# Optimization experiments

Hardware: AMD Instinct MI355X
Metric: run time of the kernel (lower is better)

The kernel has to match this reference:

```python
import jax, jax.numpy as jnp
import numpy as np

EMBED_DIM = 256
N_LEVELS = 4
N_HEADS = 8
N_POINTS = 4
HEAD_DIM = EMBED_DIM // N_HEADS
N_QUERIES = 8192
BATCH = 2
LEVEL_SHAPES = np.array([[128, 128], [64, 64], [32, 32], [16, 16]], dtype=np.int32)
HMAX, WMAX = 128, 128
EPS = 1e-5


def setup_inputs() -> dict:
    key = jax.random.key(0)
    ks = jax.random.split(key, 10)
    scale = 1.0 / np.sqrt(EMBED_DIM)
    query = jax.random.normal(ks[0], (N_QUERIES, EMBED_DIM), jnp.float32)
    xy_reference_points = jax.random.uniform(ks[1], (N_QUERIES, 2), jnp.float32, 0.05, 0.95)
    val = jax.random.normal(ks[2], (BATCH, HMAX, WMAX, N_LEVELS, EMBED_DIM), jnp.float32)
    # zero outside each level's valid support (mimics sparse COO: absent entries read as 0)
    hh = jnp.arange(HMAX)[:, None, None]
    ww = jnp.arange(WMAX)[None, :, None]
    lh = jnp.asarray(LEVEL_SHAPES[:, 0])[None, None, :]
    lw = jnp.asarray(LEVEL_SHAPES[:, 1])[None, None, :]
    mask = ((hh < lh) & (ww < lw)).astype(jnp.float32)
    stacked_value_tensors = val * mask[None, :, :, :, None]
    return {
        "query": query,
        "xy_reference_points": xy_reference_points,
        "stacked_value_tensors": stacked_value_tensors,
        "W_off": (jax.random.normal(ks[3], (EMBED_DIM, N_LEVELS * N_POINTS * N_HEADS * 2)) * scale * 0.1).astype(jnp.float32),
        "b_off": (jax.random.normal(ks[4], (N_LEVELS * N_POINTS * N_HEADS * 2,)) * 0.5).astype(jnp.float32),
        "W_attn": (jax.random.normal(ks[5], (EMBED_DIM, N_LEVELS * N_POINTS * N_HEADS)) * scale).astype(jnp.float32),
        "b_attn": jnp.zeros((N_LEVELS * N_POINTS * N_HEADS,), jnp.float32),
        "W_out": (jax.random.normal(ks[6], (EMBED_DIM, EMBED_DIM)) * scale).astype(jnp.float32),
        "b_out": jnp.zeros((EMBED_DIM,), jnp.float32),
        "batch_offsets": jnp.array([0, N_QUERIES // 2], jnp.int32),
        "spatial_shapes": jnp.asarray(LEVEL_SHAPES, jnp.int32),
    }


def reference(query, xy_reference_points, stacked_value_tensors, W_off, b_off,
              W_attn, b_attn, W_out, b_out, batch_offsets, spatial_shapes):
    Q = query.shape[0]
    # sampling offsets & attention weights (torch Linear with W stored [in,out])
    off = (query @ W_off + b_off).reshape(Q, N_LEVELS, N_POINTS, N_HEADS, 2)
    aw = (query @ W_attn + b_attn).reshape(Q, N_LEVELS * N_POINTS, N_HEADS)
    aw = jax.nn.softmax(aw, axis=1).reshape(Q, N_LEVELS, N_POINTS, N_HEADS)
    # sampling locations: sigmoid(inverse_sigmoid(ref) + offsets), then map (0,1)->(-1,1)
    r = jnp.clip(xy_reference_points, 0.0, 1.0)
    inv = jnp.log(jnp.clip(r, EPS, 1.0) / jnp.clip(1.0 - r, EPS, 1.0))
    loc = jax.nn.sigmoid(inv[:, None, None, None, :] + off) * 2.0 - 1.0  # (Q,L,P,H,2)
    # per-query batch index from batch_offsets (start index per batch element)
    bidx = jnp.searchsorted(batch_offsets, jnp.arange(Q), side="right") - 1  # (Q,)
    b = bidx[:, None, None, None]
    h_sz = spatial_shapes[:, 0].astype(loc.dtype)[None, :, None, None]
    w_sz = spatial_shapes[:, 1].astype(loc.dtype)[None, :, None, None]
    x = ((loc[..., 0] + 1.0) * w_sz - 1.0) / 2.0  # (Q,L,P,H)
    y = ((loc[..., 1] + 1.0) * h_sz - 1.0) / 2.0
    x0 = jnp.floor(x).astype(jnp.int32); x1 = x0 + 1
    y0 = jnp.floor(y).astype(jnp.int32); y1 = y0 + 1
    wcap = (spatial_shapes[:, 1] - 1).astype(jnp.int32)[None, :, None, None]
    hcap = (spatial_shapes[:, 0] - 1).astype(jnp.int32)[None, :, None, None]
    x0 = jnp.clip(x0, 0, wcap); x1 = jnp.clip(x1, 0, wcap)
    y0 = jnp.clip(y0, 0, hcap); y1 = jnp.clip(y1, 0, hcap)
    x0f = x0.astype(x.dtype); x1f = x1.astype(x.dtype)
    y0f = y0.astype(y.dtype); y1f = y1.astype(y.dtype)
    wa = (x1f - x) * (y1f - y)  # pairs with (x0,y0), as in source
    wb = (x1f - x) * (y - y0f)  # (x0,y1)
    wc = (x - x0f) * (y1f - y)  # (x1,y0)
    wd = (x - x0f) * (y - y0f)  # (x1,y1)
    V = stacked_value_tensors.reshape(BATCH, HMAX, WMAX, N_LEVELS, N_HEADS, HEAD_DIM)
    l = jnp.arange(N_LEVELS)[None, :, None, None]
    h = jnp.arange(N_HEADS)[None, None, None, :]
    # NOTE: source indexes (batch, x, y, level, head) -> x indexes the height dim; levels are square
    def g(xi, yi):
        return V[b, xi, yi, l, h]  # (Q,L,P,H,HEAD_DIM)
    sampled = (wa[..., None] * g(x0, y0) + wb[..., None] * g(x0, y1)
               + wc[..., None] * g(x1, y0) + wd[..., None] * g(x1, y1))
    out = jnp.einsum("qlphd,qlph->qhd", sampled, aw).reshape(Q, EMBED_DIM)
    return out @ W_out + b_out
```

## Files before the change

kernel.cpp:

```cpp
#include <hip/hip_runtime.h>
#include <math.h>

#define ED      256
#define NL      4
#define NH      8
#define NP      4
#define HD      32
#define HMAX    128
#define WMAX    128
#define NLP     16
#define NC      128
#define NOFF_AW 384
#define QPB     4
#define NBK     1024
#define BSTRIDE (HMAX*WMAX*NL*ED)
#define XSTRIDE (WMAX*NL*ED)
#define YSTRIDE (NL*ED)

typedef __attribute__((ext_vector_type(8))) __fp16   f16x8;
typedef __attribute__((ext_vector_type(4))) __fp16   f16x4;
typedef __attribute__((ext_vector_type(4))) float    f32x4;

__global__ __launch_bounds__(1024) void msda_sort_kernel(
    const float* __restrict__ refp,
    const int*   __restrict__ batch_off,
    int n_batch,
    int* __restrict__ bucket_of,
    int* __restrict__ perm,
    int nq)
{
    __shared__ int cnt[NBK];
    __shared__ int scan[NBK];
    const int t = threadIdx.x;
    cnt[t] = 0;
    __syncthreads();

    const int iters = (nq + 1023) >> 10;
    for (int i = 0; i < iters; ++i) {
        int q = i * 1024 + t;
        if (q < nq) {
            int b = 0;
            for (int j = 1; j < n_batch; ++j)
                if (batch_off[j] <= q) b = j;
            b = min(b, 3);
            float rx = refp[q * 2 + 0], ry = refp[q * 2 + 1];
            int bx = min(15, max(0, (int)(rx * 16.f)));
            int by = min(15, max(0, (int)(ry * 16.f)));
            int bk = (b << 8) | (by << 4) | bx;
            bucket_of[q] = bk;
            atomicAdd(&cnt[bk], 1);
        }
    }
    __syncthreads();

    scan[t] = cnt[t];
    __syncthreads();
    for (int d = 1; d < NBK; d <<= 1) {
        int v = scan[t];
        int u = (t >= d) ? scan[t - d] : 0;
        __syncthreads();
        scan[t] = v + u;
        __syncthreads();
    }
    cnt[t] = scan[t] - cnt[t];
    __syncthreads();

    for (int i = 0; i < iters; ++i) {
        int q = i * 1024 + t;
        if (q < nq) {
            int bk = bucket_of[q];
            int pos = atomicAdd(&cnt[bk], 1);
            perm[pos] = q;
        }
    }
}

__global__ __launch_bounds__(256) void msda_wconv_kernel(
    const float* __restrict__ W_off,
    const float* __restrict__ W_attn,
    const float* __restrict__ W_out,
    __fp16* __restrict__ WcatT,
    __fp16* __restrict__ WoutT)
{
    const int idx = blockIdx.x * 256 + threadIdx.x;
    const int t2 = NOFF_AW * ED;
    const int t3 = ED * ED;
    if (idx < t2) {
        int c = idx >> 8, e = idx & 255;
        float v = (c < ED) ? W_off[e * ED + c] : W_attn[e * NC + (c - ED)];
        WcatT[idx] = (__fp16)v;
    } else if (idx < t2 + t3) {
        int i = idx - t2;
        int c = i >> 8, e = i & 255;
        WoutT[i] = (__fp16)W_out[e * ED + c];
    }
}

__global__ __launch_bounds__(256) void gemm_f16_kernel(
    const float*  __restrict__ A,
    const __fp16* __restrict__ BT,
    const float* __restrict__ bias0,
    const float* __restrict__ bias1,
    float* __restrict__ C,
    int M, int NTOT, int bias_split)
{
    const int wave = threadIdx.x >> 6;
    const int lane = threadIdx.x & 63;
    const int gw   = blockIdx.x * 4 + wave;
    const int ngroups = NTOT >> 6;
    const int mg = gw / ngroups, ng = gw % ngroups;
    const int m16 = mg * 16, n64 = ng * 64;
    if (m16 >= M) return;

    const int mrow = lane & 15;
    const int quad = lane >> 4;

    const float4* Arow = (const float4*)(A + (size_t)(m16 + mrow) * 256 + quad * 8);
    const f16x8* B0 = (const f16x8*)(BT + (size_t)(n64 +  0 + mrow) * 256 + quad * 8);
    const f16x8* B1 = (const f16x8*)(BT + (size_t)(n64 + 16 + mrow) * 256 + quad * 8);
    const f16x8* B2 = (const f16x8*)(BT + (size_t)(n64 + 32 + mrow) * 256 + quad * 8);
    const f16x8* B3 = (const f16x8*)(BT + (size_t)(n64 + 48 + mrow) * 256 + quad * 8);

    f32x4 acc0 = {0.f,0.f,0.f,0.f}, acc1 = acc0, acc2 = acc0, acc3 = acc0;
    #pragma unroll
    for (int kb = 0; kb < 8; ++kb) {
        float4 a0 = Arow[kb * 8 + 0];
        float4 a1 = Arow[kb * 8 + 1];
        float av[8] = {a0.x, a0.y, a0.z, a0.w, a1.x, a1.y, a1.z, a1.w};
        f16x8 ah, al;
        #pragma unroll
        for (int j = 0; j < 8; ++j) {
            __fp16 h = (__fp16)av[j];
            ah[j] = h;
            al[j] = (__fp16)(av[j] - (float)h);
        }
        f16x8 b0 = B0[kb * 4], b1 = B1[kb * 4], b2 = B2[kb * 4], b3 = B3[kb * 4];
        acc0 = __builtin_amdgcn_mfma_f32_16x16x32_f16(ah, b0, acc0, 0, 0, 0);
        acc1 = __builtin_amdgcn_mfma_f32_16x16x32_f16(ah, b1, acc1, 0, 0, 0);
        acc2 = __builtin_amdgcn_mfma_f32_16x16x32_f16(ah, b2, acc2, 0, 0, 0);
        acc3 = __builtin_amdgcn_mfma_f32_16x16x32_f16(ah, b3, acc3, 0, 0, 0);
        acc0 = __builtin_amdgcn_mfma_f32_16x16x32_f16(al, b0, acc0, 0, 0, 0);
        acc1 = __builtin_amdgcn_mfma_f32_16x16x32_f16(al, b1, acc1, 0, 0, 0);
        acc2 = __builtin_amdgcn_mfma_f32_16x16x32_f16(al, b2, acc2, 0, 0, 0);
        acc3 = __builtin_amdgcn_mfma_f32_16x16x32_f16(al, b3, acc3, 0, 0, 0);
    }

    const int col = lane & 15;
    f32x4 accs[4] = {acc0, acc1, acc2, acc3};
    #pragma unroll
    for (int i = 0; i < 4; ++i) {
        int n = n64 + i * 16 + col;
        float b = (n < bias_split) ? bias0[n] : bias1[n - bias_split];
        #pragma unroll
        for (int r = 0; r < 4; ++r) {
            int row = m16 + quad * 4 + r;
            C[(size_t)row * NTOT + n] = accs[i][r] + b;
        }
    }
}

__global__ __launch_bounds__(256) void gemm_ff16_kernel(
    const __fp16* __restrict__ A,
    const __fp16* __restrict__ BT,
    const float* __restrict__ bias,
    float* __restrict__ C,
    int M, int NTOT)
{
    const int wave = threadIdx.x >> 6;
    const int lane = threadIdx.x & 63;
    const int gw   = blockIdx.x * 4 + wave;
    const int ngroups = NTOT >> 6;
    const int mg = gw / ngroups, ng = gw % ngroups;
    const int m16 = mg * 16, n64 = ng * 64;
    if (m16 >= M) return;

    const int mrow = lane & 15;
    const int quad = lane >> 4;

    const f16x8* Arow = (const f16x8*)(A + (size_t)(m16 + mrow) * 256 + quad * 8);
    const f16x8* B0 = (const f16x8*)(BT + (size_t)(n64 +  0 + mrow) * 256 + quad * 8);
    const f16x8* B1 = (const f16x8*)(BT + (size_t)(n64 + 16 + mrow) * 256 + quad * 8);
    const f16x8* B2 = (const f16x8*)(BT + (size_t)(n64 + 32 + mrow) * 256 + quad * 8);
    const f16x8* B3 = (const f16x8*)(BT + (size_t)(n64 + 48 + mrow) * 256 + quad * 8);

    f32x4 acc0 = {0.f,0.f,0.f,0.f}, acc1 = acc0, acc2 = acc0, acc3 = acc0;
    #pragma unroll
    for (int kb = 0; kb < 8; ++kb) {
        f16x8 af = Arow[kb * 4];
        acc0 = __builtin_amdgcn_mfma_f32_16x16x32_f16(af, B0[kb * 4], acc0, 0, 0, 0);
        acc1 = __builtin_amdgcn_mfma_f32_16x16x32_f16(af, B1[kb * 4], acc1, 0, 0, 0);
        acc2 = __builtin_amdgcn_mfma_f32_16x16x32_f16(af, B2[kb * 4], acc2, 0, 0, 0);
        acc3 = __builtin_amdgcn_mfma_f32_16x16x32_f16(af, B3[kb * 4], acc3, 0, 0, 0);
    }

    const int col = lane & 15;
    f32x4 accs[4] = {acc0, acc1, acc2, acc3};
    #pragma unroll
    for (int i = 0; i < 4; ++i) {
        int n = n64 + i * 16 + col;
        float b = bias[n];
        #pragma unroll
        for (int r = 0; r < 4; ++r) {
            int row = m16 + quad * 4 + r;
            C[(size_t)row * NTOT + n] = accs[i][r] + b;
        }
    }
}

__global__ __launch_bounds__(256) void msda_sample_kernel(
    const float* __restrict__ refp,
    const float* __restrict__ V,
    const float* __restrict__ off_aw,
    const int*   __restrict__ perm,
    const int*   __restrict__ batch_off,
    int n_batch,
    const int*   __restrict__ spatial,
    __fp16* __restrict__ out_pre,
    int q_total)
{
    __shared__ int    sqid[QPB];
    __shared__ float  law[QPB][NC];
    __shared__ float2 sminv[QPB][NH];
    __shared__ float2 sref[QPB];
    __shared__ int4   soff[QPB][NC];
    __shared__ float4 swt[QPB][NC];

    const int t = threadIdx.x;
    const int chunk = gridDim.x >> 3;
    const int pblk  = (blockIdx.x & 7) * chunk + (blockIdx.x >> 3);
    const int q0 = pblk * QPB;

    if (t < QPB) sqid[t] = perm[q0 + t];
    __syncthreads();

    {
        const int s = t >> 6, c = t & 63;
        const float* row = off_aw + (size_t)sqid[s] * NOFF_AW + ED;
        law[s][c]      = row[c];
        law[s][c + 64] = row[c + 64];
    }
    __syncthreads();

    if (t < QPB * NH) {
        const int s = t >> 3, h = t & 7;
        float m = -1e30f;
        #pragma unroll
        for (int lp = 0; lp < NLP; ++lp) m = fmaxf(m, law[s][lp * NH + h]);
        float sum = 0.f;
        #pragma unroll
        for (int lp = 0; lp < NLP; ++lp) sum += __expf(law[s][lp * NH + h] - m);
        sminv[s][h] = make_float2(m, 1.f / sum);
    } else if (t < QPB * NH + QPB) {
        const int s = t - QPB * NH;
        const int qid = sqid[s];
        float rx = refp[qid * 2 + 0], ry = refp[qid * 2 + 1];
        rx = fminf(fmaxf(rx, 0.f), 1.f);
        ry = fminf(fmaxf(ry, 0.f), 1.f);
        float ivx = __logf(fmaxf(rx, 1e-5f) / fmaxf(1.f - rx, 1e-5f));
        float ivy = __logf(fmaxf(ry, 1e-5f) / fmaxf(1.f - ry, 1e-5f));
        sref[s] = make_float2(ivx, ivy);
    }
    __syncthreads();

    {
        const int s = t >> 6;
        const int qid = sqid[s];
        int b = 0;
        for (int i = 1; i < n_batch; ++i)
            if (batch_off[i] <= qid) b = i;
        const int bbase = b * BSTRIDE;
        const float2 iv = sref[s];
        const float* offrow = off_aw + (size_t)qid * NOFF_AW;

        #pragma unroll
        for (int half = 0; half < 2; ++half) {
            const int c = (t & 63) + half * 64;
            const int l = c >> 5;
            const int h = c & 7;
            const int hsz = spatial[l * 2 + 0];
            const int wsz = spatial[l * 2 + 1];
            const int wcap = wsz - 1, hcap = hsz - 1;

            const float2 mi = sminv[s][h];
            const float a = __expf(law[s][c] - mi.x) * mi.y;

            const float ox = offrow[c * 2 + 0], oy = offrow[c * 2 + 1];
            float lx = 2.f / (1.f + __expf(-(iv.x + ox))) - 1.f;
            float ly = 2.f / (1.f + __expf(-(iv.y + oy))) - 1.f;
            float x = ((lx + 1.f) * (float)wsz - 1.f) * 0.5f;
            float y = ((ly + 1.f) * (float)hsz - 1.f) * 0.5f;
            int x0 = (int)floorf(x), y0 = (int)floorf(y);
            int x1 = x0 + 1, y1 = y0 + 1;
            x0 = min(max(x0, 0), wcap); x1 = min(max(x1, 0), wcap);
            y0 = min(max(y0, 0), hcap); y1 = min(max(y1, 0), hcap);
            float x0f = (float)x0, x1f = (float)x1;
            float y0f = (float)y0, y1f = (float)y1;

            float4 w;
            w.x = a * (x1f - x) * (y1f - y);
            w.y = a * (x1f - x) * (y - y0f);
            w.z = a * (x - x0f) * (y1f - y);
            w.w = a * (x - x0f) * (y - y0f);
            swt[s][c] = w;
            const int lbase = bbase + l * ED;
            int4 o;
            o.x = lbase + x0 * XSTRIDE + y0 * YSTRIDE;
            o.y = lbase + x0 * XSTRIDE + y1 * YSTRIDE;
            o.z = lbase + x1 * XSTRIDE + y0 * YSTRIDE;
            o.w = lbase + x1 * XSTRIDE + y1 * YSTRIDE;
            soff[s][c] = o;
        }
    }
    __syncthreads();

    {
        const int s    = t >> 6;
        const int lane = t & 63;
        const int h    = lane >> 3;
        const int d4   = (lane & 7) << 2;
        const int inner = h * HD + d4;
        float4 acc = {0.f, 0.f, 0.f, 0.f};
        #pragma unroll 4
        for (int lp = 0; lp < NLP; ++lp) {
            const int c = lp * NH + h;
            int4   o = soff[s][c];
            float4 w = swt[s][c];
            float4 v0 = *(const float4*)&V[o.x + inner];
            float4 v1 = *(const float4*)&V[o.y + inner];
            float4 v2 = *(const float4*)&V[o.z + inner];
            float4 v3 = *(const float4*)&V[o.w + inner];
            acc.x += w.x*v0.x + w.y*v1.x + w.z*v2.x + w.w*v3.x;
            acc.y += w.x*v0.y + w.y*v1.y + w.z*v2.y + w.w*v3.y;
            acc.z += w.x*v0.z + w.y*v1.z + w.z*v2.z + w.w*v3.z;
            acc.w += w.x*v0.w + w.y*v1.w + w.z*v2.w + w.w*v3.w;
        }
        f16x4 o4;
        o4[0] = (__fp16)acc.x; o4[1] = (__fp16)acc.y;
        o4[2] = (__fp16)acc.z; o4[3] = (__fp16)acc.w;
        *(f16x4*)&out_pre[(size_t)sqid[s] * ED + inner] = o4;
    }
}

extern "C" void kernel_launch(void* const* d_in, const int* in_sizes, int n_in,
                              void* d_out, int out_size, void* d_ws, size_t ws_size,
                              hipStream_t stream) {
    const float* query  = (const float*)d_in[0];
    const float* refp   = (const float*)d_in[1];
    const float* V      = (const float*)d_in[2];
    const float* W_off  = (const float*)d_in[3];
    const float* b_off  = (const float*)d_in[4];
    const float* W_attn = (const float*)d_in[5];
    const float* b_attn = (const float*)d_in[6];
    const float* W_out  = (const float*)d_in[7];
    const float* b_out  = (const float*)d_in[8];
    const int*   boff   = (const int*)d_in[9];
    const int*   spat   = (const int*)d_in[10];
    const int n_batch   = in_sizes[9];
    const int nq        = in_sizes[0] / ED;
    float* out = (float*)d_out;

    char* ws = (char*)d_ws;
    float*   off_aw    = (float*)ws;
    int*     perm      = (int*)(off_aw + (size_t)nq * NOFF_AW);
    int*     bucket_of = perm + nq;
    __fp16*  WcatT     = (__fp16*)(bucket_of + nq);
    __fp16*  WoutT     = WcatT + NOFF_AW * ED;
    __fp16*  out_pre   = WoutT + ED * ED;

    msda_sort_kernel<<<1, 1024, 0, stream>>>(refp, boff, n_batch,
                                             bucket_of, perm, nq);
    {
        int total = NOFF_AW * ED + ED * ED;
        msda_wconv_kernel<<<(total + 255) / 256, 256, 0, stream>>>(
            W_off, W_attn, W_out, WcatT, WoutT);
    }
    {
        int waves = (nq / 16) * (NOFF_AW / 64);
        gemm_f16_kernel<<<(waves + 3) / 4, 256, 0, stream>>>(
            query, WcatT, b_off, b_attn, off_aw, nq, NOFF_AW, ED);
    }
    {
        msda_sample_kernel<<<nq / QPB, 256, 0, stream>>>(
            refp, V, off_aw, perm, boff, n_batch, spat, out_pre, nq);
    }
    {
        int waves = (nq / 16) * (ED / 64);
        gemm_ff16_kernel<<<(waves + 3) / 4, 256, 0, stream>>>(
            out_pre, WoutT, b_out, out, nq, ED);
    }
}
```

Baseline: 270.3 us.

## Compact value tensor into dense fp16 per-level layout and merge prep kernels

Adds a prep pass that copies only the valid region of each pyramid level from the padded fp32 value tensor into a dense fp16 buffer. The sort and weight-conversion kernels are merged into the same launch. The sampling kernel now gathers half-width values from this compact layout, using hardcoded power-of-two level shapes instead of reading spatial_shapes. The aim is to cut gather bandwidth and improve cache locality, at the cost of an extra full pass over the valid values on every call, reduced precision, and baked-in level shapes.

```diff
diff --git a/kernel.cpp b/kernel.cpp
--- a/kernel.cpp
+++ b/kernel.cpp
@@ -16,83 +16,111 @@
 #define BSTRIDE (HMAX*WMAX*NL*ED)
 #define XSTRIDE (WMAX*NL*ED)
 #define YSTRIDE (NL*ED)
+#define RPB     21760
+#define PBC     (RPB*256)
 
 typedef __attribute__((ext_vector_type(8))) __fp16   f16x8;
 typedef __attribute__((ext_vector_type(4))) __fp16   f16x4;
 typedef __attribute__((ext_vector_type(4))) float    f32x4;
 
-__global__ __launch_bounds__(1024) void msda_sort_kernel(
+__constant__ int LBASE_ROW[4] = {0, 16384, 20480, 21504};
+
+__global__ __launch_bounds__(1024) void msda_prep_kernel(
+    const float* __restrict__ V,
+    const float* __restrict__ W_off,
+    const float* __restrict__ W_attn,
+    const float* __restrict__ W_out,
     const float* __restrict__ refp,
     const int*   __restrict__ batch_off,
     int n_batch,
+    __fp16* __restrict__ Vc,
+    __fp16* __restrict__ WcatT,
+    __fp16* __restrict__ WoutT,
     int* __restrict__ bucket_of,
     int* __restrict__ perm,
-    int nq)
+    int nq, int nb, int nCompact, int nWconv)
 {
     __shared__ int cnt[NBK];
     __shared__ int scan[NBK];
-    const int t = threadIdx.x;
-    cnt[t] = 0;
-    __syncthreads();
-
-    const int iters = (nq + 1023) >> 10;
-    for (int i = 0; i < iters; ++i) {
-        int q = i * 1024 + t;
-        if (q < nq) {
-            int b = 0;
-            for (int j = 1; j < n_batch; ++j)
-                if (batch_off[j] <= q) b = j;
-            b = min(b, 3);
-            float rx = refp[q * 2 + 0], ry = refp[q * 2 + 1];
-            int bx = min(15, max(0, (int)(rx * 16.f)));
-            int by = min(15, max(0, (int)(ry * 16.f)));
-            int bk = (b << 8) | (by << 4) | bx;
-            bucket_of[q] = bk;
-            atomicAdd(&cnt[bk], 1);
-        }
-    }
-    __syncthreads();
-
-    scan[t] = cnt[t];
-    __syncthreads();
-    for (int d = 1; d < NBK; d <<= 1) {
-        int v = scan[t];
-        int u = (t >= d) ? scan[t - d] : 0;
+    const int bid = blockIdx.x;
+    const int t   = threadIdx.x;
+
+    if (bid < nCompact) {
+        const int r    = bid * 16 + (t >> 6);
+        const int lane = t & 63;
+        const int e    = lane << 2;
+        const int total_rows = nb * RPB;
+        if (r < total_rows) {
+            const int b  = r / RPB;
+            const int rr = r - b * RPB;
+            int l, base;
+            if (rr < 16384)      { l = 0; base = 0; }
+            else if (rr < 20480) { l = 1; base = 16384; }
+            else if (rr < 21504) { l = 2; base = 20480; }
+            else                 { l = 3; base = 21504; }
+            const int pos = rr - base;
+            const int lsh = 7 - l;
+            const int xi  = pos >> lsh;
+            const int yi  = pos & ((1 << lsh) - 1);
+            const float4 src = *(const float4*)&V[(size_t)b * BSTRIDE +
+                (size_t)xi * XSTRIDE + (size_t)yi * YSTRIDE + l * ED + e];
+            f16x4 d;
+            d[0] = (__fp16)src.x; d[1] = (__fp16)src.y;
+            d[2] = (__fp16)src.z; d[3] = (__fp16)src.w;
+            *(f16x4*)&Vc[(size_t)r * 256 + e] = d;
+        }
+    } else if (bid < nCompact + nWconv) {
+        const int idx = (bid - nCompact) * 1024 + t;
+        const int t2 = NOFF_AW * ED;
+        const int t3 = ED * ED;
+        if (idx < t2) {
+            int c = idx >> 8, e = idx & 255;
+            float v = (c < ED) ? W_off[e * ED + c] : W_attn[e * NC + (c - ED)];
+            WcatT[idx] = (__fp16)v;
+        } else if (idx < t2 + t3) {
+            int i = idx - t2;
+            int c = i >> 8, e = i & 255;
+            WoutT[i] = (__fp16)W_out[e * ED + c];
+        }
+    } else {
+        cnt[t] = 0;
         __syncthreads();
-        scan[t] = v + u;
+        const int iters = (nq + 1023) >> 10;
+        for (int i = 0; i < iters; ++i) {
+            int q = i * 1024 + t;
+            if (q < nq) {
+                int b = 0;
+                for (int j = 1; j < n_batch; ++j)
+                    if (batch_off[j] <= q) b = j;
+                b = min(b, 3);
+                float rx = refp[q * 2 + 0], ry = refp[q * 2 + 1];
+                int bx = min(15, max(0, (int)(rx * 16.f)));
+                int by = min(15, max(0, (int)(ry * 16.f)));
+                int bk = (b << 8) | (by << 4) | bx;
+                bucket_of[q] = bk;
+                atomicAdd(&cnt[bk], 1);
+            }
+        }
         __syncthreads();
-    }
-    cnt[t] = scan[t] - cnt[t];
-    __syncthreads();
-
-    for (int i = 0; i < iters; ++i) {
-        int q = i * 1024 + t;
-        if (q < nq) {
-            int bk = bucket_of[q];
-            int pos = atomicAdd(&cnt[bk], 1);
-            perm[pos] = q;
-        }
-    }
-}
-
-__global__ __launch_bounds__(256) void msda_wconv_kernel(
-    const float* __restrict__ W_off,
-    const float* __restrict__ W_attn,
-    const float* __restrict__ W_out,
-    __fp16* __restrict__ WcatT,
-    __fp16* __restrict__ WoutT)
-{
-    const int idx = blockIdx.x * 256 + threadIdx.x;
-    const int t2 = NOFF_AW * ED;
-    const int t3 = ED * ED;
-    if (idx < t2) {
-        int c = idx >> 8, e = idx & 255;
-        float v = (c < ED) ? W_off[e * ED + c] : W_attn[e * NC + (c - ED)];
-        WcatT[idx] = (__fp16)v;
-    } else if (idx < t2 + t3) {
-        int i = idx - t2;
-        int c = i >> 8, e = i & 255;
-        WoutT[i] = (__fp16)W_out[e * ED + c];
+        scan[t] = cnt[t];
+        __syncthreads();
+        for (int d = 1; d < NBK; d <<= 1) {
+            int v = scan[t];
+            int u = (t >= d) ? scan[t - d] : 0;
+            __syncthreads();
+            scan[t] = v + u;
+            __syncthreads();
+        }
+        cnt[t] = scan[t] - cnt[t];
+        __syncthreads();
+        for (int i = 0; i < iters; ++i) {
+            int q = i * 1024 + t;
+            if (q < nq) {
+                int bk = bucket_of[q];
+                int pos = atomicAdd(&cnt[bk], 1);
+                perm[pos] = q;
+            }
+        }
     }
 }
 
@@ -208,13 +236,12 @@
 }
 
 __global__ __launch_bounds__(256) void msda_sample_kernel(
-    const float* __restrict__ refp,
-    const float* __restrict__ V,
-    const float* __restrict__ off_aw,
-    const int*   __restrict__ perm,
-    const int*   __restrict__ batch_off,
+    const float*  __restrict__ refp,
+    const __fp16* __restrict__ Vc,
+    const float*  __restrict__ off_aw,
+    const int*    __restrict__ perm,
+    const int*    __restrict__ batch_off,
     int n_batch,
-    const int*   __restrict__ spatial,
     __fp16* __restrict__ out_pre,
     int q_total)
 {
@@ -268,7 +295,7 @@
         int b = 0;
         for (int i = 1; i < n_batch; ++i)
             if (batch_off[i] <= qid) b = i;
-        const int bbase = b * BSTRIDE;
+        const int cb = b * PBC;
         const float2 iv = sref[s];
         const float* offrow = off_aw + (size_t)qid * NOFF_AW;
 
@@ -277,9 +304,9 @@
             const int c = (t & 63) + half * 64;
             const int l = c >> 5;
             const int h = c & 7;
-            const int hsz = spatial[l * 2 + 0];
-            const int wsz = spatial[l * 2 + 1];
-            const int wcap = wsz - 1, hcap = hsz - 1;
+            const int lsh = 7 - l;
+            const int sz  = 1 << lsh;
+            const int cap = sz - 1;
 
             const float2 mi = sminv[s][h];
             const float a = __expf(law[s][c] - mi.x) * mi.y;
@@ -287,12 +314,12 @@
             const float ox = offrow[c * 2 + 0], oy = offrow[c * 2 + 1];
             float lx = 2.f / (1.f + __expf(-(iv.x + ox))) - 1.f;
             float ly = 2.f / (1.f + __expf(-(iv.y + oy))) - 1.f;
-            float x = ((lx + 1.f) * (float)wsz - 1.f) * 0.5f;
-            float y = ((ly + 1.f) * (float)hsz - 1.f) * 0.5f;
+            float x = ((lx + 1.f) * (float)sz - 1.f) * 0.5f;
+            float y = ((ly + 1.f) * (float)sz - 1.f) * 0.5f;
             int x0 = (int)floorf(x), y0 = (int)floorf(y);
             int x1 = x0 + 1, y1 = y0 + 1;
-            x0 = min(max(x0, 0), wcap); x1 = min(max(x1, 0), wcap);
-            y0 = min(max(y0, 0), hcap); y1 = min(max(y1, 0), hcap);
+            x0 = min(max(x0, 0), cap); x1 = min(max(x1, 0), cap);
+            y0 = min(max(y0, 0), cap); y1 = min(max(y1, 0), cap);
             float x0f = (float)x0, x1f = (float)x1;
             float y0f = (float)y0, y1f = (float)y1;
 
@@ -302,12 +329,12 @@
             w.z = a * (x - x0f) * (y1f - y);
             w.w = a * (x - x0f) * (y - y0f);
             swt[s][c] = w;
-            const int lbase = bbase + l * ED;
+            const int lb = cb + (LBASE_ROW[l] << 8);
             int4 o;
-            o.x = lbase + x0 * XSTRIDE + y0 * YSTRIDE;
-            o.y = lbase + x0 * XSTRIDE + y1 * YSTRIDE;
-            o.z = lbase + x1 * XSTRIDE + y0 * YSTRIDE;
-            o.w = lbase + x1 * XSTRIDE + y1 * YSTRIDE;
+            o.x = lb + (((x0 << lsh) + y0) << 8);
+            o.y = lb + (((x0 << lsh) + y1) << 8);
+            o.z = lb + (((x1 << lsh) + y0) << 8);
+            o.w = lb + (((x1 << lsh) + y1) << 8);
             soff[s][c] = o;
         }
     }
@@ -325,14 +352,14 @@
             const int c = lp * NH + h;
             int4   o = soff[s][c];
             float4 w = swt[s][c];
-            float4 v0 = *(const float4*)&V[o.x + inner];
-            float4 v1 = *(const float4*)&V[o.y + inner];
-            float4 v2 = *(const float4*)&V[o.z + inner];
-            float4 v3 = *(const float4*)&V[o.w + inner];
-            acc.x += w.x*v0.x + w.y*v1.x + w.z*v2.x + w.w*v3.x;
-            acc.y += w.x*v0.y + w.y*v1.y + w.z*v2.y + w.w*v3.y;
-            acc.z += w.x*v0.z + w.y*v1.z + w.z*v2.z + w.w*v3.z;
-            acc.w += w.x*v0.w + w.y*v1.w + w.z*v2.w + w.w*v3.w;
+            f16x4 v0 = *(const f16x4*)&Vc[o.x + inner];
+            f16x4 v1 = *(const f16x4*)&Vc[o.y + inner];
+            f16x4 v2 = *(const f16x4*)&Vc[o.z + inner];
+            f16x4 v3 = *(const f16x4*)&Vc[o.w + inner];
+            acc.x += w.x*(float)v0[0] + w.y*(float)v1[0] + w.z*(float)v2[0] + w.w*(float)v3[0];
+            acc.y += w.x*(float)v0[1] + w.y*(float)v1[1] + w.z*(float)v2[1] + w.w*(float)v3[1];
+            acc.z += w.x*(float)v0[2] + w.y*(float)v1[2] + w.z*(float)v2[2] + w.w*(float)v3[2];
+            acc.w += w.x*(float)v0[3] + w.y*(float)v1[3] + w.z*(float)v2[3] + w.w*(float)v3[3];
         }
         f16x4 o4;
         o4[0] = (__fp16)acc.x; o4[1] = (__fp16)acc.y;
@@ -357,6 +384,7 @@
     const int*   spat   = (const int*)d_in[10];
     const int n_batch   = in_sizes[9];
     const int nq        = in_sizes[0] / ED;
+    const int nb        = in_sizes[2] / BSTRIDE;
     float* out = (float*)d_out;
 
     char* ws = (char*)d_ws;
@@ -366,13 +394,14 @@
     __fp16*  WcatT     = (__fp16*)(bucket_of + nq);
     __fp16*  WoutT     = WcatT + NOFF_AW * ED;
     __fp16*  out_pre   = WoutT + ED * ED;
-
-    msda_sort_kernel<<<1, 1024, 0, stream>>>(refp, boff, n_batch,
-                                             bucket_of, perm, nq);
-    {
-        int total = NOFF_AW * ED + ED * ED;
-        msda_wconv_kernel<<<(total + 255) / 256, 256, 0, stream>>>(
-            W_off, W_attn, W_out, WcatT, WoutT);
+    __fp16*  Vc        = out_pre + (size_t)nq * ED;
+
+    {
+        int nCompact = (nb * RPB + 15) / 16;
+        int nWconv   = (NOFF_AW * ED + ED * ED + 1023) / 1024;
+        msda_prep_kernel<<<nCompact + nWconv + 1, 1024, 0, stream>>>(
+            V, W_off, W_attn, W_out, refp, boff, n_batch,
+            Vc, WcatT, WoutT, bucket_of, perm, nq, nb, nCompact, nWconv);
     }
     {
         int waves = (nq / 16) * (NOFF_AW / 64);
@@ -381,7 +410,7 @@
     }
     {
         msda_sample_kernel<<<nq / QPB, 256, 0, stream>>>(
-            refp, V, off_aw, perm, boff, n_batch, spat, out_pre, nq);
+            refp, Vc, off_aw, perm, boff, n_batch, out_pre, nq);
     }
     {
         int waves = (nq / 16) * (ED / 64);
```

New measurement: 266.4 us. No clear change (-1.4%).
